# Kernel optimization log

Hardware: AMD Instinct MI355X
Metric: run time of the kernel (lower is better)

Reference implementation:

```python
import jax, jax.numpy as jnp
import numpy as np

N_ENT = 100000
N_REL = 500
D = 50
N_EDGES = 2000000


def segment_softmax(scores, seg, n):
    # numerically stable softmax over edges grouped by segment id
    m = jax.ops.segment_max(scores, seg, num_segments=n)
    m = jnp.where(jnp.isfinite(m), m, 0.0)
    e = jnp.exp(scores - m[seg])
    s = jax.ops.segment_sum(e, seg, num_segments=n)
    return e / (s[seg] + 1e-9)


def kbgat(h, r, t, E, R, W, a, Wr, relation_relu, n_ent):
    # relation transform
    rel = R @ Wr
    if relation_relu:
        rel = jax.nn.relu(rel)
    d = E.shape[1]
    # per-triple feature: concat(E[h], R[r], E[t]) @ W, computed without materializing the concat
    feat = E[h] @ W[:d] + R[r] @ W[d:2 * d] + E[t] @ W[2 * d:]  # [n_edges, units]
    score = jax.nn.leaky_relu(feat @ a, 0.2)                      # [n_edges]
    alpha = segment_softmax(score, h, n_ent)                      # softmax over neighbors of each head entity
    out = jax.ops.segment_sum(alpha[:, None] * feat, h, num_segments=n_ent)  # [n_ent, units]
    return out, rel


def setup_inputs() -> dict:
    key = jax.random.key(0)
    ks = jax.random.split(key, 14)
    std = np.sqrt(1.0 / D).astype(np.float32)
    h_index = jax.random.randint(ks[0], (N_EDGES,), 0, N_ENT, dtype=jnp.int32)
    r_index = jax.random.randint(ks[1], (N_EDGES,), 0, N_REL, dtype=jnp.int32)
    t_index = jax.random.randint(ks[2], (N_EDGES,), 0, N_ENT, dtype=jnp.int32)
    E = jax.random.normal(ks[3], (N_ENT, D), dtype=jnp.float32) * std
    R = jax.random.normal(ks[4], (N_REL, D), dtype=jnp.float32) * std
    g = lambda k, shape, fan: jax.random.normal(k, shape, dtype=jnp.float32) * np.sqrt(1.0 / fan).astype(np.float32)
    W0 = g(ks[5], (3 * D, D), 3 * D)
    a0 = g(ks[6], (D,), D)
    Wr0 = g(ks[7], (D, D), D)
    W1 = g(ks[8], (3 * D, D), 3 * D)
    a1 = g(ks[9], (D,), D)
    Wr1 = g(ks[10], (D, D), D)
    Wd = g(ks[11], (D, D), D)
    bd = jnp.zeros((D,), dtype=jnp.float32)
    return {"h_index": h_index, "r_index": r_index, "t_index": t_index,
            "E": E, "R": R, "W0": W0, "a0": a0, "Wr0": Wr0,
            "W1": W1, "a1": a1, "Wr1": Wr1, "Wd": Wd, "bd": bd}


def reference(h_index, r_index, t_index, E, R, W0, a0, Wr0, W1, a1, Wr1, Wd, bd):
    # dropout rate = 0 -> identity. num_heads = 1 -> concat / add_n are identities.
    e0, rel0 = kbgat(h_index, r_index, t_index, E, R, W0, a0, Wr0, True, N_ENT)
    e1, rel1 = kbgat(h_index, r_index, t_index, e0, rel0, W1, a1, Wr1, False, N_ENT)
    entity_features = e1 + E @ Wd + bd  # residual dense on original entity embeddings
    return entity_features, rel1
```

## Files before the change

### kernel.cpp

```cpp
#include <hip/hip_runtime.h>

#define N_ENT   100000
#define N_REL   500
#define DD      50
#define LD      52
#define LD2     64
#define LDH     64
#define N_EDGES 2000000
#define T_BITS  17
#define T_MASK  0x1FFFF
#define BBITS   9
#define BMASK   511
#define NB      196
#define CHUNK   4096
#define SSH     14
#define SSTRIDE (1 << SSH)
#define ENT_BLOCKS   2500
#define BKT_BLOCKS   489
#define REL_BLOCKS   100

typedef float v2f __attribute__((ext_vector_type(2)));

__device__ inline unsigned int pack_bf2(float x, float y) {
    unsigned int xu = __float_as_uint(x);
    unsigned int yu = __float_as_uint(y);
    xu = (xu + 0x7FFFu + ((xu >> 16) & 1u)) >> 16;
    yu = (yu + 0x7FFFu + ((yu >> 16) & 1u)) >> 16;
    return xu | (yu << 16);
}
__device__ inline v2f unpk2(unsigned int v) {
    v2f r;
    r.x = __uint_as_float(v << 16);
    r.y = __uint_as_float(v & 0xFFFF0000u);
    return r;
}

template<int NMAT>
__device__ void ent_pre_body(float* smemF, int bid,
    const float* __restrict__ X, int ldX,
    const float* __restrict__ Wa,
    const float* __restrict__ Wb,
    const float* __restrict__ Wc,
    const float* __restrict__ bd,
    const float* __restrict__ avec,
    float* __restrict__ Ya,
    unsigned short* __restrict__ Ybh,
    float* __restrict__ Yc,
    float* __restrict__ shOut,
    float* __restrict__ stOut)
{
    constexpr int MT = 40;
    float* sW = smemF;
    float* sX = sW + NMAT * DD * DD;
    float* sY = sX + MT * 52;
    float* sa = sY + MT * 52;

    const int tid = threadIdx.x;

    for (int i = tid; i < DD * DD / 4; i += 512) {
        ((float4*)sW)[i] = ((const float4*)Wa)[i];
        ((float4*)(sW + DD * DD))[i] = ((const float4*)Wb)[i];
        if (NMAT == 3) ((float4*)(sW + 2 * DD * DD))[i] = ((const float4*)Wc)[i];
    }
    if (tid < DD) sa[tid] = avec[tid];

    const int m0 = bid * MT;
    const int nX4 = MT * ldX / 4;
    const float4* xsrc = (const float4*)(X + (size_t)m0 * ldX);
    for (int i = tid; i < nX4; i += 512) ((float4*)sX)[i] = xsrc[i];
    __syncthreads();

    const bool active = (tid < 500);
    const int mp = active ? tid / 25 : 0;
    const int jp = active ? tid % 25 : 0;
    const int r0 = 2 * mp, r1 = 2 * mp + 1, j0 = 2 * jp;

    float acc[NMAT][2][2];
    #pragma unroll
    for (int t = 0; t < NMAT; t++)
        #pragma unroll
        for (int i = 0; i < 2; i++)
            #pragma unroll
            for (int c = 0; c < 2; c++) acc[t][i][c] = 0.f;

    if (active) {
        if (NMAT == 3) {
            float b0 = bd[j0], b1 = bd[j0 + 1];
            acc[2][0][0] = b0; acc[2][0][1] = b1;
            acc[2][1][0] = b0; acc[2][1][1] = b1;
        }
        const float* xr0 = &sX[r0 * ldX];
        const float* xr1 = &sX[r1 * ldX];
        for (int k = 0; k < DD; k++) {
            float x0 = xr0[k], x1 = xr1[k];
            #pragma unroll
            for (int t = 0; t < NMAT; t++) {
                float2 w = *(const float2*)&sW[t * DD * DD + k * DD + j0];
                acc[t][0][0] += x0 * w.x; acc[t][0][1] += x0 * w.y;
                acc[t][1][0] += x1 * w.x; acc[t][1][1] += x1 * w.y;
            }
        }
    }

    if (tid < MT * 2) sY[(tid >> 1) * 52 + 50 + (tid & 1)] = 0.f;

    if (active) {
        sY[r0 * 52 + j0]     = acc[0][0][0];
        sY[r0 * 52 + j0 + 1] = acc[0][0][1];
        sY[r1 * 52 + j0]     = acc[0][1][0];
        sY[r1 * 52 + j0 + 1] = acc[0][1][1];
    }
    __syncthreads();
    {
        float4* dst = (float4*)(Ya + (size_t)m0 * LD);
        for (int i = tid; i < MT * LD / 4; i += 512) dst[i] = ((const float4*)sY)[i];
        if (tid < MT) {
            const float* row = &sY[tid * 52];
            float d = 0.f;
            for (int k = 0; k < DD; k++) d += row[k] * sa[k];
            shOut[m0 + tid] = d;
        }
    }
    __syncthreads();

    unsigned int* sYhU = (unsigned int*)sX;
    if (active) {
        sY[r0 * 52 + j0]     = acc[1][0][0];
        sY[r0 * 52 + j0 + 1] = acc[1][0][1];
        sY[r1 * 52 + j0]     = acc[1][1][0];
        sY[r1 * 52 + j0 + 1] = acc[1][1][1];
        sYhU[r0 * 32 + jp] = pack_bf2(acc[1][0][0], acc[1][0][1]);
        sYhU[r1 * 32 + jp] = pack_bf2(acc[1][1][0], acc[1][1][1]);
    }
    if (tid < MT * 7) sYhU[(tid / 7) * 32 + 25 + (tid % 7)] = 0u;
    __syncthreads();
    {
        float4* dst = (float4*)(Ybh + (size_t)m0 * LDH);
        for (int i = tid; i < MT * LDH * 2 / 16; i += 512) dst[i] = ((const float4*)sYhU)[i];
        if (tid < MT) {
            const float* row = &sY[tid * 52];
            float d = 0.f;
            for (int k = 0; k < DD; k++) d += row[k] * sa[k];
            stOut[m0 + tid] = d;
        }
    }

    if (NMAT == 3) {
        __syncthreads();
        if (active) {
            sY[r0 * 52 + j0]     = acc[2][0][0];
            sY[r0 * 52 + j0 + 1] = acc[2][0][1];
            sY[r1 * 52 + j0]     = acc[2][1][0];
            sY[r1 * 52 + j0 + 1] = acc[2][1][1];
        }
        __syncthreads();
        float4* dst = (float4*)(Yc + (size_t)m0 * LD);
        for (int i = tid; i < MT * LD / 4; i += 512) dst[i] = ((const float4*)sY)[i];
    }
}

template<int NMAT>
__global__ __launch_bounds__(512) void ent_pre_v6(
    const float* __restrict__ X, int ldX,
    const float* __restrict__ Wa,
    const float* __restrict__ Wb,
    const float* __restrict__ Wc,
    const float* __restrict__ bd,
    const float* __restrict__ avec,
    float* __restrict__ Ya,
    unsigned short* __restrict__ Ybh,
    float* __restrict__ Yc,
    float* __restrict__ shOut,
    float* __restrict__ stOut)
{
    __shared__ __align__(16) float smemF[NMAT * DD * DD + 40 * 52 * 2 + 64];
    ent_pre_body<NMAT>(smemF, blockIdx.x, X, ldX, Wa, Wb, Wc, bd, avec,
                       Ya, Ybh, Yc, shOut, stOut);
}

__device__ void rel_body(float* smemF, int bid,
    const float* __restrict__ Rin, int ld_in,
    const float* __restrict__ Wr,
    const float* __restrict__ Wmid,
    const float* __restrict__ avec,
    int do_relu,
    float* __restrict__ rel_out, int ld_rel,
    float* __restrict__ RW_out,
    float* __restrict__ sr)
{
    float* sWr  = smemF;
    float* sWm  = sWr + DD * DD;
    float* sRed = sWm + DD * DD;

    for (int i = threadIdx.x; i < DD * DD; i += blockDim.x) {
        sWr[i] = Wr[i];
        sWm[i] = Wmid[i];
    }
    __syncthreads();
    const int tid = threadIdx.x;
    const bool act = (tid < 250);
    const int m = bid * 5 + tid / 50;
    const int j = tid % 50;
    float am = 0.f;
    if (act) {
        const float* x = Rin + (size_t)m * ld_in;
        float ar = 0.f;
        for (int k = 0; k < DD; k++) {
            float xv = x[k];
            ar += xv * sWr[k * DD + j];
            am += xv * sWm[k * DD + j];
        }
        if (do_relu) ar = fmaxf(ar, 0.f);
        rel_out[(size_t)m * ld_rel + j] = ar;
        RW_out[(size_t)m * LD2 + j] = am;
        if (j < LD2 - DD) RW_out[(size_t)m * LD2 + DD + j] = 0.f;
    }
    if (tid < 256) sRed[tid] = act ? am * avec[j] : 0.f;
    __syncthreads();
    if (tid < 5) {
        float d = 0.f;
        const float* p = &sRed[tid * 50];
        for (int k = 0; k < 50; k++) d += p[k];
        sr[bid * 5 + tid] = d;
    }
}


__device__ void bucket_body(float* smemF, int bid,
    const int* __restrict__ h,
    const int* __restrict__ r,
    const int* __restrict__ t,
    int* __restrict__ ccur,
    unsigned int* __restrict__ stagedP,
    unsigned short* __restrict__ stagedH, int nE)
{
    int* sHist = (int*)smemF;
    int* sScan = sHist + NB;
    int* sBase = sScan + 512;
    int* sCur  = sBase + NB;
    int* sGb   = sCur + NB;
    unsigned int*   sPay = (unsigned int*)(sGb + NB);
    unsigned short* sLoc = (unsigned short*)(sPay + CHUNK);
    unsigned char*  sBkt = (unsigned char*)(sLoc + CHUNK);

    const int tid = threadIdx.x;
    const int e0 = bid * CHUNK;
    const int n = min(CHUNK, nE - e0);

    for (int i = tid; i < NB; i += 512) sHist[i] = 0;
    __syncthreads();

    #pragma unroll
    for (int k = 0; k < CHUNK / 512; k++) {
        int e = e0 + k * 512 + tid;
        if (e < nE) atomicAdd(&sHist[h[e] >> BBITS], 1);
    }
    __syncthreads();

    int v = (tid < NB) ? sHist[tid] : 0;
    sScan[tid] = v;
    __syncthreads();
    for (int off = 1; off < 512; off <<= 1) {
        int x = (tid >= off) ? sScan[tid - off] : 0;
        __syncthreads();
        sScan[tid] += x;
        __syncthreads();
    }
    if (tid < NB) {
        int excl = sScan[tid] - v;
        sBase[tid] = excl;
        sCur[tid] = excl;
    }
    __syncthreads();

    #pragma unroll
    for (int k = 0; k < CHUNK / 512; k++) {
        int e = e0 + k * 512 + tid;
        if (e < nE) {
            int hv = h[e];
            int b = hv >> BBITS;
            int pos = atomicAdd(&sCur[b], 1);
            sPay[pos] = ((unsigned int)r[e] << T_BITS) | (unsigned int)t[e];
            sLoc[pos] = (unsigned short)(hv & BMASK);
            sBkt[pos] = (unsigned char)b;
        }
    }
    __syncthreads();

    if (tid < NB) {
        int cnt = sHist[tid];
        sGb[tid] = (tid << SSH) + (cnt ? atomicAdd(&ccur[tid], cnt) : 0);
    }
    __syncthreads();

    for (int i = tid; i < n; i += 512) {
        int b = sBkt[i];
        int g = sGb[b] + (i - sBase[b]);
        stagedP[g] = sPay[i];
        stagedH[g] = sLoc[i];
    }
}

__global__ __launch_bounds__(512) void bkt_rel0_kernel(
    const int* __restrict__ h,
    const int* __restrict__ r,
    const int* __restrict__ t,
    int* __restrict__ ccur,
    unsigned int* __restrict__ stagedP,
    unsigned short* __restrict__ stagedH, int nE,
    const float* __restrict__ R,
    const float* __restrict__ Wr0,
    const float* __restrict__ Wmid0,
    const float* __restrict__ a0,
    float* __restrict__ rel0,
    float* __restrict__ RW,
    float* __restrict__ sr)
{
    __shared__ __align__(16) float smemF[8480];
    if (blockIdx.x < BKT_BLOCKS) {
        bucket_body(smemF, blockIdx.x, h, r, t, ccur, stagedP, stagedH, nE);
    } else {
        rel_body(smemF, blockIdx.x - BKT_BLOCKS, R, DD, Wr0, Wmid0, a0, 1,
                 rel0, LD, RW, sr);
    }
}

__device__ void final_scatter_body(float* smemF, int b,
    const unsigned int* __restrict__ stagedP,
    const unsigned short* __restrict__ stagedH,
    const int* __restrict__ ccnt,
    int* __restrict__ counts,
    int* __restrict__ s0,
    unsigned int* __restrict__ rtp)
{
    int* sCnt  = (int*)smemF;
    int* sScan = sCnt + 512;
    int* sOff  = sScan + 512;

    const int i0 = b << SSH;
    const int i1 = i0 + ccnt[b];
    const int tid = threadIdx.x;

    sCnt[tid] = 0;
    __syncthreads();

    for (int i = i0 + tid; i < i1; i += 512)
        atomicAdd(&sCnt[stagedH[i]], 1);
    __syncthreads();

    const int v = sCnt[tid];
    sScan[tid] = v;
    __syncthreads();
    for (int off = 1; off < 512; off <<= 1) {
        int x = (tid >= off) ? sScan[tid - off] : 0;
        __syncthreads();
        sScan[tid] += x;
        __syncthreads();
    }
    const int excl = sScan[tid] - v;
    sOff[tid] = excl;

    const int u = (b << BBITS) + tid;
    if (u < N_ENT) {
        counts[u] = v;
        s0[u] = i0 + excl;
    }
    __syncthreads();

    for (int i = i0 + tid; i < i1; i += 512) {
        unsigned int p = stagedP[i];
        int loc = stagedH[i];
        int pos = i0 + atomicAdd(&sOff[loc], 1);
        rtp[pos] = p;
    }
}

__global__ __launch_bounds__(512) void fse_rel1_kernel(
    const unsigned int* __restrict__ stagedP,
    const unsigned short* __restrict__ stagedH,
    const int* __restrict__ ccnt,
    int* __restrict__ counts,
    int* __restrict__ s0,
    unsigned int* __restrict__ rtp,
    const float* __restrict__ E,
    const float* __restrict__ W0,
    const float* __restrict__ Wd,
    const float* __restrict__ bd,
    const float* __restrict__ a0,
    float* __restrict__ EW1,
    unsigned short* __restrict__ EW3h,
    float* __restrict__ Ed,
    float* __restrict__ sh,
    float* __restrict__ st,
    const float* __restrict__ rel0,
    const float* __restrict__ Wr1,
    const float* __restrict__ Wmid1,
    const float* __restrict__ a1,
    float* __restrict__ out_rel,
    float* __restrict__ RW1,
    float* __restrict__ sr1)
{
    __shared__ __align__(16) float smemF[3 * DD * DD + 40 * 52 * 2 + 64];
    if (blockIdx.x < NB) {
        final_scatter_body(smemF, blockIdx.x, stagedP, stagedH, ccnt,
                           counts, s0, rtp);
    } else if (blockIdx.x < NB + ENT_BLOCKS) {
        ent_pre_body<3>(smemF, blockIdx.x - NB, E, DD,
                        W0, W0 + 2 * DD * DD, Wd, bd, a0,
                        EW1, EW3h, Ed, sh, st);
    } else {
        rel_body(smemF, blockIdx.x - NB - ENT_BLOCKS, rel0, LD,
                 Wr1, Wmid1, a1, 0, out_rel, DD, RW1, sr1);
    }
}

__global__ __launch_bounds__(256) void accum_fused_kernel(
    const int* __restrict__ s0v,
    const int* __restrict__ counts,
    const unsigned int* __restrict__ rtp,
    const float* __restrict__ sh,
    const float* __restrict__ sr,
    const float* __restrict__ st,
    const float* __restrict__ EW1,
    const float* __restrict__ RW,
    const unsigned short* __restrict__ EW3h,
    const float* __restrict__ base,
    float* __restrict__ outp, int full_ld)
{
    const int wid = (blockIdx.x * blockDim.x + threadIdx.x) >> 6;
    if (2 * wid >= N_ENT) return;
    const int lane  = threadIdx.x & 63;
    const int half  = lane >> 5;
    const int hlane = lane & 31;
    const int eg = hlane >> 3;
    const int q  = hlane & 7;
    const int sbase = half << 5;
    const unsigned qh = (unsigned)q << 4;
    const unsigned qr = (unsigned)q << 5;

    const int u = 2 * wid + half;
    const int b = s0v[u];
    const int c = counts[u];
    const float shu = sh[u];

    const char* __restrict__ pH = (const char*)EW3h;
    const char* __restrict__ pR = (const char*)RW;
    const char* __restrict__ pS = (const char*)sr;
    const char* __restrict__ pT = (const char*)st;

    v2f acc2[4];
    #pragma unroll
    for (int k = 0; k < 4; k++) { acc2[k].x = 0.f; acc2[k].y = 0.f; }
    float asum = 0.f;

    for (int i0 = 0; i0 < c; i0 += 32) {
        const int cb = min(32, c - i0);
        const int e = i0 + hlane;
        const unsigned w = rtp[b + min(e, c - 1)];
        float ex = 0.f;
        if (e < c) {
            float srv = *(const float*)(pS + ((w >> T_BITS) << 2));
            float stv = *(const float*)(pT + ((w & T_MASK) << 2));
            float sc = shu + srv + stv;
            sc = sc >= 0.f ? sc : 0.2f * sc;
            ex = __expf(sc);
        }
        asum += ex;

        const int nst = (cb + 3) >> 2;

#define LOADSTEP(S, TH, VA, VB, EX) {                                   \
        const int _src = sbase + min((S) * 4 + eg, cb - 1);             \
        const unsigned _wv = (unsigned)__shfl((int)w, _src);            \
        EX = __shfl(ex, _src);                                          \
        const unsigned _oH = ((_wv & T_MASK) << 7) | qh;                \
        const unsigned _oR = ((_wv >> T_BITS) << 8) | qr;               \
        TH = *(const uint4*)(pH + _oH);                                 \
        VA = *(const float4*)(pR + _oR);                                \
        VB = *(const float4*)(pR + _oR + 16); }

        uint4 th0, th1; float4 va0, vb0, va1, vb1; float ex0, ex1;
        LOADSTEP(0, th0, va0, vb0, ex0)
        LOADSTEP(1, th1, va1, vb1, ex1)

        for (int s = 0; s < nst; s++) {
            uint4 thn; float4 van, vbn; float exn;
            LOADSTEP(s + 2, thn, van, vbn, exn)

            const float exv = (s * 4 + eg < cb) ? ex0 : 0.f;
            v2f ex2; ex2.x = exv; ex2.y = exv;
            v2f p01; p01.x = va0.x; p01.y = va0.y;
            v2f p23; p23.x = va0.z; p23.y = va0.w;
            v2f p45; p45.x = vb0.x; p45.y = vb0.y;
            v2f p67; p67.x = vb0.z; p67.y = vb0.w;
            acc2[0] += ex2 * (p01 + unpk2(th0.x));
            acc2[1] += ex2 * (p23 + unpk2(th0.y));
            acc2[2] += ex2 * (p45 + unpk2(th0.z));
            acc2[3] += ex2 * (p67 + unpk2(th0.w));

            th0 = th1; va0 = va1; vb0 = vb1; ex0 = ex1;
            th1 = thn; va1 = van; vb1 = vbn; ex1 = exn;
        }
#undef LOADSTEP
    }

    const int ej = 8 * hlane;
    const bool ep = (hlane < 8) && (ej < LD);
    const bool efull = ep && (ej < 48);
    float4 w1a, w1b, ba, bb;
    if (ep) {
        const float* e1 = EW1 + (size_t)u * LD + (efull ? ej : 48);
        w1a = *(const float4*)e1;
        if (efull) w1b = *(const float4*)(e1 + 4);
        if (base) {
            const float* bp = base + (size_t)u * LD + (efull ? ej : 48);
            ba = *(const float4*)bp;
            if (efull) bb = *(const float4*)(bp + 4);
        }
    }

    float acc[8];
    #pragma unroll
    for (int k = 0; k < 4; k++) { acc[2 * k] = acc2[k].x; acc[2 * k + 1] = acc2[k].y; }
    #pragma unroll
    for (int off = 16; off >= 8; off >>= 1) {
        #pragma unroll
        for (int k = 0; k < 8; k++) acc[k] += __shfl_down(acc[k], off, 32);
        asum += __shfl_down(asum, off, 32);
    }
    asum += __shfl_xor(asum, 4);
    asum += __shfl_xor(asum, 2);
    asum += __shfl_xor(asum, 1);

    if (hlane >= 8) return;
    const int j0 = 8 * hlane;
    if (j0 >= LD) return;

    if (asum > 0.f) {
        float inv = 1.f / asum;
        if (j0 < 48) {
            acc[0] = w1a.x + acc[0] * inv; acc[1] = w1a.y + acc[1] * inv;
            acc[2] = w1a.z + acc[2] * inv; acc[3] = w1a.w + acc[3] * inv;
            acc[4] = w1b.x + acc[4] * inv; acc[5] = w1b.y + acc[5] * inv;
            acc[6] = w1b.z + acc[6] * inv; acc[7] = w1b.w + acc[7] * inv;
        } else {
            acc[0] = w1a.x + acc[0] * inv; acc[1] = w1a.y + acc[1] * inv;
            acc[2] = w1a.z + acc[2] * inv; acc[3] = w1a.w + acc[3] * inv;
        }
    }
    if (base) {
        if (j0 < 48) {
            acc[0] += ba.x; acc[1] += ba.y; acc[2] += ba.z; acc[3] += ba.w;
            acc[4] += bb.x; acc[5] += bb.y; acc[6] += bb.z; acc[7] += bb.w;
        } else {
            acc[0] += ba.x; acc[1] += ba.y; acc[2] += ba.z; acc[3] += ba.w;
        }
    }
    if (full_ld) {
        if (j0 < 48) {
            *(float4*)(outp + (size_t)u * LD + j0) =
                make_float4(acc[0], acc[1], acc[2], acc[3]);
            *(float4*)(outp + (size_t)u * LD + j0 + 4) =
                make_float4(acc[4], acc[5], acc[6], acc[7]);
        } else {
            *(float4*)(outp + (size_t)u * LD + 48) =
                make_float4(acc[0], acc[1], acc[2], acc[3]);
        }
    } else {
        float* row = outp + (size_t)u * DD;
        if (j0 < 48) {
            *(float2*)(row + j0)     = make_float2(acc[0], acc[1]);
            *(float2*)(row + j0 + 2) = make_float2(acc[2], acc[3]);
            *(float2*)(row + j0 + 4) = make_float2(acc[4], acc[5]);
            *(float2*)(row + j0 + 6) = make_float2(acc[6], acc[7]);
        } else {
            *(float2*)(row + 48) = make_float2(acc[0], acc[1]);
        }
    }
}

extern "C" void kernel_launch(void* const* d_in, const int* in_sizes, int n_in,
                              void* d_out, int out_size, void* d_ws, size_t ws_size,
                              hipStream_t stream)
{
    const int*   h   = (const int*)d_in[0];
    const int*   r   = (const int*)d_in[1];
    const int*   t   = (const int*)d_in[2];
    const float* E   = (const float*)d_in[3];
    const float* R   = (const float*)d_in[4];
    const float* W0  = (const float*)d_in[5];
    const float* a0  = (const float*)d_in[6];
    const float* Wr0 = (const float*)d_in[7];
    const float* W1  = (const float*)d_in[8];
    const float* a1  = (const float*)d_in[9];
    const float* Wr1 = (const float*)d_in[10];
    const float* Wd  = (const float*)d_in[11];
    const float* bd  = (const float*)d_in[12];

    float* out_ent = (float*)d_out;
    float* out_rel = out_ent + (size_t)N_ENT * DD;

    float* ws_f  = (float*)d_ws;
    float* EW1   = ws_f;
    float* Ed    = EW1  + (size_t)N_ENT * LD;
    float* e0    = Ed   + (size_t)N_ENT * LD;
    unsigned short* EW3h = (unsigned short*)(e0 + (size_t)N_ENT * LD);
    float* RW    = (float*)(EW3h + (size_t)N_ENT * LDH);
    float* RW1   = RW   + (size_t)N_REL * LD2;
    float* rel0  = RW1  + (size_t)N_REL * LD2;
    float* sh    = rel0 + (size_t)N_REL * LD;
    float* st    = sh   + N_ENT;
    float* sr    = st   + N_ENT;
    float* sr1   = sr   + N_REL;
    int* counts  = (int*)(sr1 + N_REL);
    int* s0      = counts + N_ENT;
    int* ccur    = s0 + N_ENT;
    unsigned int* rtp    = (unsigned int*)(ccur + NB);
    unsigned int*   stagedP = (unsigned int*)e0;
    unsigned short* stagedH = (unsigned short*)(stagedP + (size_t)NB * SSTRIDE);

    const int BLK = 256;
    const int gW  = (N_ENT / 2 + 3) / 4;

    hipMemsetAsync(ccur, 0, (size_t)NB * sizeof(int), stream);
    bkt_rel0_kernel<<<BKT_BLOCKS + REL_BLOCKS, 512, 0, stream>>>(
        h, r, t, ccur, stagedP, stagedH, N_EDGES,
        R, Wr0, W0 + DD * DD, a0, rel0, RW, sr);

    fse_rel1_kernel<<<NB + ENT_BLOCKS + REL_BLOCKS, 512, 0, stream>>>(
        stagedP, stagedH, ccur, counts, s0, rtp,
        E, W0, Wd, bd, a0, EW1, EW3h, Ed, sh, st,
        rel0, Wr1, W1 + DD * DD, a1, out_rel, RW1, sr1);

    accum_fused_kernel<<<gW, BLK, 0, stream>>>(s0, counts, rtp, sh, sr, st,
                                               EW1, RW, EW3h, nullptr, e0, 1);

    ent_pre_v6<2><<<ENT_BLOCKS, 512, 0, stream>>>(e0, LD, W1, W1 + 2 * DD * DD,
                                                  nullptr, nullptr, a1,
                                                  EW1, EW3h, nullptr, sh, st);

    accum_fused_kernel<<<gW, BLK, 0, stream>>>(s0, counts, rtp, sh, sr1, st,
                                               EW1, RW1, EW3h, Ed, out_ent, 0);
}
```

Baseline: 336.6 us.

## Rebalance kernel fusion and split layer-0 accumulation to overlap with layer-1 precompute

```diff
diff --git a/kernel.cpp b/kernel.cpp
--- a/kernel.cpp
+++ b/kernel.cpp
@@ -18,6 +18,9 @@
 #define ENT_BLOCKS   2500
 #define BKT_BLOCKS   489
 #define REL_BLOCKS   100
+#define UHALF   50000
+#define ACCB    3125
+#define E1HB    1250
 
 typedef float v2f __attribute__((ext_vector_type(2)));
 
@@ -164,18 +167,16 @@
     const float* __restrict__ X, int ldX,
     const float* __restrict__ Wa,
     const float* __restrict__ Wb,
-    const float* __restrict__ Wc,
-    const float* __restrict__ bd,
     const float* __restrict__ avec,
     float* __restrict__ Ya,
     unsigned short* __restrict__ Ybh,
-    float* __restrict__ Yc,
     float* __restrict__ shOut,
-    float* __restrict__ stOut)
+    float* __restrict__ stOut,
+    int bid_base)
 {
     __shared__ __align__(16) float smemF[NMAT * DD * DD + 40 * 52 * 2 + 64];
-    ent_pre_body<NMAT>(smemF, blockIdx.x, X, ldX, Wa, Wb, Wc, bd, avec,
-                       Ya, Ybh, Yc, shOut, stOut);
+    ent_pre_body<NMAT>(smemF, blockIdx.x + bid_base, X, ldX, Wa, Wb,
+                       nullptr, nullptr, avec, Ya, Ybh, nullptr, shOut, stOut);
 }
 
 __device__ void rel_body(float* smemF, int bid,
@@ -225,7 +226,6 @@
     }
 }
 
-
 __device__ void bucket_body(float* smemF, int bid,
     const int* __restrict__ h,
     const int* __restrict__ r,
@@ -301,87 +301,13 @@
     }
 }
 
-__global__ __launch_bounds__(512) void bkt_rel0_kernel(
+__global__ __launch_bounds__(512) void bke_kernel(
     const int* __restrict__ h,
     const int* __restrict__ r,
     const int* __restrict__ t,
     int* __restrict__ ccur,
     unsigned int* __restrict__ stagedP,
     unsigned short* __restrict__ stagedH, int nE,
-    const float* __restrict__ R,
-    const float* __restrict__ Wr0,
-    const float* __restrict__ Wmid0,
-    const float* __restrict__ a0,
-    float* __restrict__ rel0,
-    float* __restrict__ RW,
-    float* __restrict__ sr)
-{
-    __shared__ __align__(16) float smemF[8480];
-    if (blockIdx.x < BKT_BLOCKS) {
-        bucket_body(smemF, blockIdx.x, h, r, t, ccur, stagedP, stagedH, nE);
-    } else {
-        rel_body(smemF, blockIdx.x - BKT_BLOCKS, R, DD, Wr0, Wmid0, a0, 1,
-                 rel0, LD, RW, sr);
-    }
-}
-
-__device__ void final_scatter_body(float* smemF, int b,
-    const unsigned int* __restrict__ stagedP,
-    const unsigned short* __restrict__ stagedH,
-    const int* __restrict__ ccnt,
-    int* __restrict__ counts,
-    int* __restrict__ s0,
-    unsigned int* __restrict__ rtp)
-{
-    int* sCnt  = (int*)smemF;
-    int* sScan = sCnt + 512;
-    int* sOff  = sScan + 512;
-
-    const int i0 = b << SSH;
-    const int i1 = i0 + ccnt[b];
-    const int tid = threadIdx.x;
-
-    sCnt[tid] = 0;
-    __syncthreads();
-
-    for (int i = i0 + tid; i < i1; i += 512)
-        atomicAdd(&sCnt[stagedH[i]], 1);
-    __syncthreads();
-
-    const int v = sCnt[tid];
-    sScan[tid] = v;
-    __syncthreads();
-    for (int off = 1; off < 512; off <<= 1) {
-        int x = (tid >= off) ? sScan[tid - off] : 0;
-        __syncthreads();
-        sScan[tid] += x;
-        __syncthreads();
-    }
-    const int excl = sScan[tid] - v;
-    sOff[tid] = excl;
-
-    const int u = (b << BBITS) + tid;
-    if (u < N_ENT) {
-        counts[u] = v;
-        s0[u] = i0 + excl;
-    }
-    __syncthreads();
-
-    for (int i = i0 + tid; i < i1; i += 512) {
-        unsigned int p = stagedP[i];
-        int loc = stagedH[i];
-        int pos = i0 + atomicAdd(&sOff[loc], 1);
-        rtp[pos] = p;
-    }
-}
-
-__global__ __launch_bounds__(512) void fse_rel1_kernel(
-    const unsigned int* __restrict__ stagedP,
-    const unsigned short* __restrict__ stagedH,
-    const int* __restrict__ ccnt,
-    int* __restrict__ counts,
-    int* __restrict__ s0,
-    unsigned int* __restrict__ rtp,
     const float* __restrict__ E,
     const float* __restrict__ W0,
     const float* __restrict__ Wd,
@@ -392,6 +318,83 @@
     float* __restrict__ Ed,
     float* __restrict__ sh,
     float* __restrict__ st,
+    const float* __restrict__ R,
+    const float* __restrict__ Wr0,
+    const float* __restrict__ Wmid0,
+    float* __restrict__ rel0,
+    float* __restrict__ RW,
+    float* __restrict__ sr)
+{
+    __shared__ __align__(16) float smemF[3 * DD * DD + 40 * 52 * 2 + 64];
+    if (blockIdx.x < BKT_BLOCKS) {
+        bucket_body(smemF, blockIdx.x, h, r, t, ccur, stagedP, stagedH, nE);
+    } else if (blockIdx.x < BKT_BLOCKS + ENT_BLOCKS) {
+        ent_pre_body<3>(smemF, blockIdx.x - BKT_BLOCKS, E, DD,
+                        W0, W0 + 2 * DD * DD, Wd, bd, a0,
+                        EW1, EW3h, Ed, sh, st);
+    } else {
+        rel_body(smemF, blockIdx.x - BKT_BLOCKS - ENT_BLOCKS, R, DD,
+                 Wr0, Wmid0, a0, 1, rel0, LD, RW, sr);
+    }
+}
+
+__device__ void final_scatter_body(float* smemF, int b,
+    const unsigned int* __restrict__ stagedP,
+    const unsigned short* __restrict__ stagedH,
+    const int* __restrict__ ccnt,
+    int* __restrict__ counts,
+    int* __restrict__ s0,
+    unsigned int* __restrict__ rtp)
+{
+    int* sCnt  = (int*)smemF;
+    int* sScan = sCnt + 512;
+    int* sOff  = sScan + 512;
+
+    const int i0 = b << SSH;
+    const int i1 = i0 + ccnt[b];
+    const int tid = threadIdx.x;
+
+    sCnt[tid] = 0;
+    __syncthreads();
+
+    for (int i = i0 + tid; i < i1; i += 512)
+        atomicAdd(&sCnt[stagedH[i]], 1);
+    __syncthreads();
+
+    const int v = sCnt[tid];
+    sScan[tid] = v;
+    __syncthreads();
+    for (int off = 1; off < 512; off <<= 1) {
+        int x = (tid >= off) ? sScan[tid - off] : 0;
+        __syncthreads();
+        sScan[tid] += x;
+        __syncthreads();
+    }
+    const int excl = sScan[tid] - v;
+    sOff[tid] = excl;
+
+    const int u = (b << BBITS) + tid;
+    if (u < N_ENT) {
+        counts[u] = v;
+        s0[u] = i0 + excl;
+    }
+    __syncthreads();
+
+    for (int i = i0 + tid; i < i1; i += 512) {
+        unsigned int p = stagedP[i];
+        int loc = stagedH[i];
+        int pos = i0 + atomicAdd(&sOff[loc], 1);
+        rtp[pos] = p;
+    }
+}
+
+__global__ __launch_bounds__(512) void fs_rel1_kernel(
+    const unsigned int* __restrict__ stagedP,
+    const unsigned short* __restrict__ stagedH,
+    const int* __restrict__ ccnt,
+    int* __restrict__ counts,
+    int* __restrict__ s0,
+    unsigned int* __restrict__ rtp,
     const float* __restrict__ rel0,
     const float* __restrict__ Wr1,
     const float* __restrict__ Wmid1,
@@ -400,21 +403,17 @@
     float* __restrict__ RW1,
     float* __restrict__ sr1)
 {
-    __shared__ __align__(16) float smemF[3 * DD * DD + 40 * 52 * 2 + 64];
+    __shared__ __align__(16) float smemF[2 * DD * DD + 256 + 16];
     if (blockIdx.x < NB) {
         final_scatter_body(smemF, blockIdx.x, stagedP, stagedH, ccnt,
                            counts, s0, rtp);
-    } else if (blockIdx.x < NB + ENT_BLOCKS) {
-        ent_pre_body<3>(smemF, blockIdx.x - NB, E, DD,
-                        W0, W0 + 2 * DD * DD, Wd, bd, a0,
-                        EW1, EW3h, Ed, sh, st);
     } else {
-        rel_body(smemF, blockIdx.x - NB - ENT_BLOCKS, rel0, LD,
-                 Wr1, Wmid1, a1, 0, out_rel, DD, RW1, sr1);
-    }
-}
-
-__global__ __launch_bounds__(256) void accum_fused_kernel(
+        rel_body(smemF, blockIdx.x - NB, rel0, LD, Wr1, Wmid1, a1, 0,
+                 out_rel, DD, RW1, sr1);
+    }
+}
+
+__device__ void accum_body(int u,
     const int* __restrict__ s0v,
     const int* __restrict__ counts,
     const unsigned int* __restrict__ rtp,
@@ -427,8 +426,6 @@
     const float* __restrict__ base,
     float* __restrict__ outp, int full_ld)
 {
-    const int wid = (blockIdx.x * blockDim.x + threadIdx.x) >> 6;
-    if (2 * wid >= N_ENT) return;
     const int lane  = threadIdx.x & 63;
     const int half  = lane >> 5;
     const int hlane = lane & 31;
@@ -438,7 +435,6 @@
     const unsigned qh = (unsigned)q << 4;
     const unsigned qr = (unsigned)q << 5;
 
-    const int u = 2 * wid + half;
     const int b = s0v[u];
     const int c = counts[u];
     const float shu = sh[u];
@@ -576,6 +572,58 @@
         } else {
             *(float2*)(row + 48) = make_float2(acc[0], acc[1]);
         }
+    }
+}
+
+__global__ __launch_bounds__(256) void accum_fused_kernel(
+    const int* __restrict__ s0v,
+    const int* __restrict__ counts,
+    const unsigned int* __restrict__ rtp,
+    const float* __restrict__ sh,
+    const float* __restrict__ sr,
+    const float* __restrict__ st,
+    const float* __restrict__ EW1,
+    const float* __restrict__ RW,
+    const unsigned short* __restrict__ EW3h,
+    const float* __restrict__ base,
+    float* __restrict__ outp, int full_ld,
+    int ubase, int ucount)
+{
+    const int wid = (blockIdx.x * blockDim.x + threadIdx.x) >> 6;
+    if (2 * wid >= ucount) return;
+    const int u = ubase + 2 * wid + ((threadIdx.x >> 5) & 1);
+    accum_body(u, s0v, counts, rtp, sh, sr, st, EW1, RW, EW3h,
+               base, outp, full_ld);
+}
+
+__global__ __launch_bounds__(512) void acc_ent_kernel(
+    const int* __restrict__ s0v,
+    const int* __restrict__ counts,
+    const unsigned int* __restrict__ rtp,
+    const float* __restrict__ sh,
+    const float* __restrict__ sr,
+    const float* __restrict__ st,
+    const float* __restrict__ EW1,
+    const float* __restrict__ RW,
+    const unsigned short* __restrict__ EW3h,
+    float* __restrict__ e0,
+    const float* __restrict__ W1a,
+    const float* __restrict__ W1c,
+    const float* __restrict__ a1,
+    unsigned short* __restrict__ EW3hb,
+    float* __restrict__ sh1,
+    float* __restrict__ st1)
+{
+    __shared__ __align__(16) float smemF[2 * DD * DD + 40 * 52 * 2 + 64];
+    if (blockIdx.x < ACCB) {
+        const int wid = (blockIdx.x * 512 + threadIdx.x) >> 6;
+        const int u = UHALF + 2 * wid + ((threadIdx.x >> 5) & 1);
+        accum_body(u, s0v, counts, rtp, sh, sr, st, EW1, RW, EW3h,
+                   nullptr, e0, 1);
+    } else {
+        ent_pre_body<2>(smemF, blockIdx.x - ACCB, e0, LD, W1a, W1c,
+                        nullptr, nullptr, a1,
+                        (float*)EW1, EW3hb, nullptr, sh1, st1);
     }
 }
 
@@ -616,29 +664,49 @@
     int* s0      = counts + N_ENT;
     int* ccur    = s0 + N_ENT;
     unsigned int* rtp    = (unsigned int*)(ccur + NB);
+    unsigned short* EW3hb = (unsigned short*)(rtp + (size_t)NB * SSTRIDE);
+    float* sh1   = (float*)(EW3hb + (size_t)N_ENT * LDH);
+    float* st1   = sh1 + N_ENT;
+    const size_t needA = (size_t)((char*)(st1 + N_ENT) - (char*)d_ws);
+    const bool split = (ws_size >= needA);
+    if (!split) {
+        EW3hb = EW3h;
+        sh1 = sh;
+        st1 = st;
+    }
     unsigned int*   stagedP = (unsigned int*)e0;
     unsigned short* stagedH = (unsigned short*)(stagedP + (size_t)NB * SSTRIDE);
 
     const int BLK = 256;
-    const int gW  = (N_ENT / 2 + 3) / 4;
 
     hipMemsetAsync(ccur, 0, (size_t)NB * sizeof(int), stream);
-    bkt_rel0_kernel<<<BKT_BLOCKS + REL_BLOCKS, 512, 0, stream>>>(
+    bke_kernel<<<BKT_BLOCKS + ENT_BLOCKS + REL_BLOCKS, 512, 0, stream>>>(
         h, r, t, ccur, stagedP, stagedH, N_EDGES,
-        R, Wr0, W0 + DD * DD, a0, rel0, RW, sr);
-
-    fse_rel1_kernel<<<NB + ENT_BLOCKS + REL_BLOCKS, 512, 0, stream>>>(
+        E, W0, Wd, bd, a0, EW1, EW3h, Ed, sh, st,
+        R, Wr0, W0 + DD * DD, rel0, RW, sr);
+
+    fs_rel1_kernel<<<NB + REL_BLOCKS, 512, 0, stream>>>(
         stagedP, stagedH, ccur, counts, s0, rtp,
-        E, W0, Wd, bd, a0, EW1, EW3h, Ed, sh, st,
         rel0, Wr1, W1 + DD * DD, a1, out_rel, RW1, sr1);
 
-    accum_fused_kernel<<<gW, BLK, 0, stream>>>(s0, counts, rtp, sh, sr, st,
-                                               EW1, RW, EW3h, nullptr, e0, 1);
-
-    ent_pre_v6<2><<<ENT_BLOCKS, 512, 0, stream>>>(e0, LD, W1, W1 + 2 * DD * DD,
-                                                  nullptr, nullptr, a1,
-                                                  EW1, EW3h, nullptr, sh, st);
-
-    accum_fused_kernel<<<gW, BLK, 0, stream>>>(s0, counts, rtp, sh, sr1, st,
-                                               EW1, RW1, EW3h, Ed, out_ent, 0);
-}
+    if (split) {
+        accum_fused_kernel<<<UHALF / 8, BLK, 0, stream>>>(
+            s0, counts, rtp, sh, sr, st, EW1, RW, EW3h, nullptr, e0, 1,
+            0, UHALF);
+        acc_ent_kernel<<<ACCB + E1HB, 512, 0, stream>>>(
+            s0, counts, rtp, sh, sr, st, EW1, RW, EW3h, e0,
+            W1, W1 + 2 * DD * DD, a1, EW3hb, sh1, st1);
+        ent_pre_v6<2><<<E1HB, 512, 0, stream>>>(
+            e0, LD, W1, W1 + 2 * DD * DD, a1, EW1, EW3hb, sh1, st1, E1HB);
+    } else {
+        accum_fused_kernel<<<N_ENT / 8, BLK, 0, stream>>>(
+            s0, counts, rtp, sh, sr, st, EW1, RW, EW3h, nullptr, e0, 1,
+            0, N_ENT);
+        ent_pre_v6<2><<<ENT_BLOCKS, 512, 0, stream>>>(
+            e0, LD, W1, W1 + 2 * DD * DD, a1, EW1, EW3hb, sh1, st1, 0);
+    }
+
+    accum_fused_kernel<<<N_ENT / 8, BLK, 0, stream>>>(
+        s0, counts, rtp, sh1, sr1, st1, EW1, RW1, EW3hb, Ed, out_ent, 0,
+        0, N_ENT);
+}
```

Result: slower. 386.5 us (+14.8%).

## Double entity rows per block in ent_pre and compute four rows per thread

Applied to the files above, without the earlier changes.

```diff
diff --git a/kernel.cpp b/kernel.cpp
--- a/kernel.cpp
+++ b/kernel.cpp
@@ -15,7 +15,7 @@
 #define CHUNK   4096
 #define SSH     14
 #define SSTRIDE (1 << SSH)
-#define ENT_BLOCKS   2500
+#define ENT_BLOCKS   1250
 #define BKT_BLOCKS   489
 #define REL_BLOCKS   100
 
@@ -49,7 +49,7 @@
     float* __restrict__ shOut,
     float* __restrict__ stOut)
 {
-    constexpr int MT = 40;
+    constexpr int MT = 80;
     float* sW = smemF;
     float* sX = sW + NMAT * DD * DD;
     float* sY = sX + MT * 52;
@@ -73,31 +73,35 @@
     const bool active = (tid < 500);
     const int mp = active ? tid / 25 : 0;
     const int jp = active ? tid % 25 : 0;
-    const int r0 = 2 * mp, r1 = 2 * mp + 1, j0 = 2 * jp;
-
-    float acc[NMAT][2][2];
+    const int r0 = 4 * mp, j0 = 2 * jp;
+
+    float acc[NMAT][4][2];
     #pragma unroll
     for (int t = 0; t < NMAT; t++)
         #pragma unroll
-        for (int i = 0; i < 2; i++)
-            #pragma unroll
-            for (int c = 0; c < 2; c++) acc[t][i][c] = 0.f;
+        for (int i = 0; i < 4; i++) {
+            acc[t][i][0] = 0.f; acc[t][i][1] = 0.f;
+        }
 
     if (active) {
         if (NMAT == 3) {
             float b0 = bd[j0], b1 = bd[j0 + 1];
-            acc[2][0][0] = b0; acc[2][0][1] = b1;
-            acc[2][1][0] = b0; acc[2][1][1] = b1;
-        }
-        const float* xr0 = &sX[r0 * ldX];
-        const float* xr1 = &sX[r1 * ldX];
+            #pragma unroll
+            for (int i = 0; i < 4; i++) { acc[2][i][0] = b0; acc[2][i][1] = b1; }
+        }
+        const float* xr = &sX[r0 * ldX];
         for (int k = 0; k < DD; k++) {
-            float x0 = xr0[k], x1 = xr1[k];
+            float x0 = xr[k];
+            float x1 = xr[k + ldX];
+            float x2 = xr[k + 2 * ldX];
+            float x3 = xr[k + 3 * ldX];
             #pragma unroll
             for (int t = 0; t < NMAT; t++) {
                 float2 w = *(const float2*)&sW[t * DD * DD + k * DD + j0];
                 acc[t][0][0] += x0 * w.x; acc[t][0][1] += x0 * w.y;
                 acc[t][1][0] += x1 * w.x; acc[t][1][1] += x1 * w.y;
+                acc[t][2][0] += x2 * w.x; acc[t][2][1] += x2 * w.y;
+                acc[t][3][0] += x3 * w.x; acc[t][3][1] += x3 * w.y;
             }
         }
     }
@@ -105,10 +109,11 @@
     if (tid < MT * 2) sY[(tid >> 1) * 52 + 50 + (tid & 1)] = 0.f;
 
     if (active) {
-        sY[r0 * 52 + j0]     = acc[0][0][0];
-        sY[r0 * 52 + j0 + 1] = acc[0][0][1];
-        sY[r1 * 52 + j0]     = acc[0][1][0];
-        sY[r1 * 52 + j0 + 1] = acc[0][1][1];
+        #pragma unroll
+        for (int i = 0; i < 4; i++) {
+            sY[(r0 + i) * 52 + j0]     = acc[0][i][0];
+            sY[(r0 + i) * 52 + j0 + 1] = acc[0][i][1];
+        }
     }
     __syncthreads();
     {
@@ -125,14 +130,15 @@
 
     unsigned int* sYhU = (unsigned int*)sX;
     if (active) {
-        sY[r0 * 52 + j0]     = acc[1][0][0];
-        sY[r0 * 52 + j0 + 1] = acc[1][0][1];
-        sY[r1 * 52 + j0]     = acc[1][1][0];
-        sY[r1 * 52 + j0 + 1] = acc[1][1][1];
-        sYhU[r0 * 32 + jp] = pack_bf2(acc[1][0][0], acc[1][0][1]);
-        sYhU[r1 * 32 + jp] = pack_bf2(acc[1][1][0], acc[1][1][1]);
-    }
-    if (tid < MT * 7) sYhU[(tid / 7) * 32 + 25 + (tid % 7)] = 0u;
+        #pragma unroll
+        for (int i = 0; i < 4; i++) {
+            sY[(r0 + i) * 52 + j0]     = acc[1][i][0];
+            sY[(r0 + i) * 52 + j0 + 1] = acc[1][i][1];
+            sYhU[(r0 + i) * 32 + jp] = pack_bf2(acc[1][i][0], acc[1][i][1]);
+        }
+    }
+    for (int i = tid; i < MT * 7; i += 512)
+        sYhU[(i / 7) * 32 + 25 + (i % 7)] = 0u;
     __syncthreads();
     {
         float4* dst = (float4*)(Ybh + (size_t)m0 * LDH);
@@ -148,10 +154,11 @@
     if (NMAT == 3) {
         __syncthreads();
         if (active) {
-            sY[r0 * 52 + j0]     = acc[2][0][0];
-            sY[r0 * 52 + j0 + 1] = acc[2][0][1];
-            sY[r1 * 52 + j0]     = acc[2][1][0];
-            sY[r1 * 52 + j0 + 1] = acc[2][1][1];
+            #pragma unroll
+            for (int i = 0; i < 4; i++) {
+                sY[(r0 + i) * 52 + j0]     = acc[2][i][0];
+                sY[(r0 + i) * 52 + j0 + 1] = acc[2][i][1];
+            }
         }
         __syncthreads();
         float4* dst = (float4*)(Yc + (size_t)m0 * LD);
@@ -173,7 +180,7 @@
     float* __restrict__ shOut,
     float* __restrict__ stOut)
 {
-    __shared__ __align__(16) float smemF[NMAT * DD * DD + 40 * 52 * 2 + 64];
+    __shared__ __align__(16) float smemF[NMAT * DD * DD + 80 * 52 * 2 + 64];
     ent_pre_body<NMAT>(smemF, blockIdx.x, X, ldX, Wa, Wb, Wc, bd, avec,
                        Ya, Ybh, Yc, shOut, stOut);
 }
@@ -400,7 +407,7 @@
     float* __restrict__ RW1,
     float* __restrict__ sr1)
 {
-    __shared__ __align__(16) float smemF[3 * DD * DD + 40 * 52 * 2 + 64];
+    __shared__ __align__(16) float smemF[3 * DD * DD + 80 * 52 * 2 + 64];
     if (blockIdx.x < NB) {
         final_scatter_body(smemF, blockIdx.x, stagedP, stagedH, ccnt,
                            counts, s0, rtp);
```

After: 312.8 us. 7.1% less time.
